# Kernel optimization log

Hardware: AMD Instinct MI355X
Metric: run time of the kernel (lower is better)

Reference implementation:

```python
import jax, jax.numpy as jnp
import numpy as np
import math

HEADS = 8


def rope(t):
    # t: [..., seq, dim]; lucidrains-style interleaved rotary embedding
    seq, dim = t.shape[-2], t.shape[-1]
    inv = 1.0 / (10000.0 ** (jnp.arange(0, dim, 2, dtype=jnp.float32) / dim))
    freqs = jnp.arange(seq, dtype=jnp.float32)[:, None] * inv[None, :]  # [seq, dim/2]
    freqs = jnp.repeat(freqs, 2, axis=-1)                               # [seq, dim]
    cos, sin = jnp.cos(freqs), jnp.sin(freqs)
    t2 = t.reshape(t.shape[:-1] + (dim // 2, 2))
    rot = jnp.stack([-t2[..., 1], t2[..., 0]], axis=-1).reshape(t.shape)
    return t * cos + rot * sin


def conv1x3(x, w):
    # x: [b,c,h,w], w: [out_c,in_c,1,3], padding (0,1), no bias
    return jax.lax.conv_general_dilated(
        x, w, window_strides=(1, 1), padding=((0, 0), (1, 1)),
        dimension_numbers=('NCHW', 'OIHW', 'NCHW'))


def mcl_pw(x, w_pw):
    # per-channel linear on feature axis h: w_pw [c, out_f, in_f]
    return jnp.einsum('bchw,cgh->bcgw', x, w_pw)


def setup_inputs() -> dict:
    key = jax.random.key(0)
    ks = jax.random.split(key, 10)
    b, c, f, w = 2, 8, 256, 1024
    s = 0.05
    return {
        'x': jax.random.normal(ks[0], (b, c, f, w), dtype=jnp.float32),
        'q_pw': jax.random.normal(ks[1], (c, f, f), dtype=jnp.float32) * s,
        'q_cw': jax.random.normal(ks[2], (c, c, 1, 3), dtype=jnp.float32) * s,
        'k_pw': jax.random.normal(ks[3], (c, f, f), dtype=jnp.float32) * s,
        'k_cw': jax.random.normal(ks[4], (c, c, 1, 3), dtype=jnp.float32) * s,
        'v_pw': jax.random.normal(ks[5], (c, f, f), dtype=jnp.float32) * s,
        'v_cw': jax.random.normal(ks[6], (c, c, 1, 3), dtype=jnp.float32) * s,
        'out_pw': jax.random.normal(ks[7], (c, f, f), dtype=jnp.float32) * s,
        'out_dw': jax.random.normal(ks[8], (c, c), dtype=jnp.float32) * s,
    }


def reference(x, q_pw, q_cw, k_pw, k_cw, v_pw, v_cw, out_pw, out_dw):
    b, c, h, w = x.shape
    hd = h // HEADS

    def split_heads(y):  # [b,c,h,w] -> [b,c,heads,w,hd]
        return y.transpose(0, 1, 3, 2).reshape(b, c, w, HEADS, hd).transpose(0, 1, 3, 2, 4)

    q = rope(split_heads(conv1x3(mcl_pw(x, q_pw), q_cw)))
    k = rope(split_heads(conv1x3(mcl_pw(x, k_pw), k_cw)))
    v = split_heads(conv1x3(mcl_pw(x, v_pw), v_cw))

    # non-standard scaling by sqrt(h) = sqrt(features)
    qk = jnp.einsum('bcnqd,bcnkd->bcnqk', q, k) / math.sqrt(h)
    a = jnp.einsum('bcnqk,bcnkd->bcnqd', jax.nn.softmax(qk, axis=-1), v)
    a = a.transpose(0, 1, 3, 2, 4).reshape(b, c, w, h).transpose(0, 1, 3, 2)  # [b,c,h,w]

    # out_proj: depthwise channel mix then per-channel positionwise linear
    out = jnp.einsum('bchw,dc->bdhw', a, out_dw)
    out = mcl_pw(out, out_pw)
    return out
```

## Files before the change

### kernel.cpp

```cpp
#include <hip/hip_runtime.h>
#include <hip/hip_bf16.h>

#define B 2
#define C 8
#define F 256
#define W 1024
#define NH 8
#define HD 32

typedef float f32x4 __attribute__((ext_vector_type(4)));
typedef short sh8 __attribute__((ext_vector_type(8)));
typedef short sh4 __attribute__((ext_vector_type(4)));
typedef unsigned short u16;

static __device__ __forceinline__ u16 f2b(float x) {
  union { __hip_bfloat16 h; u16 u; } v;
  v.h = __float2bfloat16(x);
  return v.u;
}
static __device__ __forceinline__ float b2f(u16 x) {
  union { unsigned int u; float f; } v;
  v.u = ((unsigned int)x) << 16;
  return v.f;
}
static __device__ __forceinline__ float ubits(unsigned int u) {
  union { unsigned int u; float f; } v;
  v.u = u;
  return v.f;
}

static __device__ __forceinline__ f32x4 mfma32(sh8 a, sh8 b, f32x4 c) {
  return __builtin_amdgcn_mfma_f32_16x16x32_bf16(a, b, c, 0, 0, 0);
}

static __device__ __forceinline__ f32x4 mfma16(sh4 a, sh4 b, f32x4 c) {
#if __has_builtin(__builtin_amdgcn_mfma_f32_16x16x16bf16_1k)
  return __builtin_amdgcn_mfma_f32_16x16x16bf16_1k(a, b, c, 0, 0, 0);
#else
  f32x4 d;
  asm("v_mfma_f32_16x16x16_bf16 %0, %1, %2, %3" : "=v"(d) : "v"(a), "v"(b), "v"(c));
  return d;
#endif
}

static __device__ __forceinline__ void gload16(const u16* g, u16* l, int ln) {
#if __has_builtin(__builtin_amdgcn_global_load_lds)
  __builtin_amdgcn_global_load_lds((const __attribute__((address_space(1))) void*)g,
                                   (__attribute__((address_space(3))) void*)l, 16, 0, 0);
#else
  *(sh8*)(l + ln * 8) = *(const sh8*)g;
#endif
}

__global__ __launch_bounds__(256) void cvt4(const float* __restrict__ s0, const float* __restrict__ s1,
                                            const float* __restrict__ s2, const float* __restrict__ s3,
                                            u16* __restrict__ d0, u16* __restrict__ d1,
                                            u16* __restrict__ d2, u16* __restrict__ d3, int n4) {
  const int which = blockIdx.y;
  const float* s = which == 0 ? s0 : which == 1 ? s1 : which == 2 ? s2 : s3;
  u16* d = which == 0 ? d0 : which == 1 ? d1 : which == 2 ? d2 : d3;
  const int i = blockIdx.x * 256 + threadIdx.x;
  if (i < n4) {
    const float4 v = reinterpret_cast<const float4*>(s)[i];
    union { u16 h[4]; uint2 u; } o;
    o.h[0] = f2b(v.x); o.h[1] = f2b(v.y); o.h[2] = f2b(v.z); o.h[3] = f2b(v.w);
    reinterpret_cast<uint2*>(d)[i] = o.u;
  }
}

__global__ __launch_bounds__(256) void rope_tab_k(float2* __restrict__ TAB) {
  const int idx = blockIdx.x * 256 + threadIdx.x;
  const int j = idx >> 10, w = idx & 1023;
  const float inv = powf(10000.f, -(float)(2 * j) / 32.f);
  float sn, cs;
  sincosf((float)w * inv, &sn, &cs);
  TAB[idx] = make_float2(cs, sn);
}

__global__ __launch_bounds__(256) void xt_k(const float* __restrict__ x,
                                            u16* __restrict__ xt) {
  const int bc = blockIdx.z, h0 = blockIdx.y * 32, w0 = blockIdx.x * 32;
  const int t = threadIdx.x;
  __shared__ u16 sm[32][34];
  const int a = t & 31, bql = t >> 5;
  const float* src = x + ((size_t)bc * F + h0) * W + w0;
#pragma unroll
  for (int p = 0; p < 4; ++p) {
    const int hl = bql + p * 8;
    sm[a][hl] = f2b(src[(size_t)hl * W + a]);
  }
  __syncthreads();
  u16* dst = xt + ((size_t)bc * W + w0) * F + h0;
#pragma unroll
  for (int p = 0; p < 4; ++p) {
    const int wl = bql + p * 8;
    dst[(size_t)wl * F + a] = sm[wl][a];
  }
}

template <bool OUTBF>
__global__ __launch_bounds__(256) void gemm_bt(const u16* __restrict__ Aw,
                                               const u16* __restrict__ Bt,
                                               void* __restrict__ Cc) {
  const int bc = blockIdx.z;
  const int proj = blockIdx.y >> 1;
  const int g0 = (blockIdx.y & 1) * 128;
  const int w0 = blockIdx.x * 64;
  const int t = threadIdx.x;
  const int ln = t & 63, wid = t >> 6;
  const int lr = ln & 15, lk = (ln >> 4) * 8;
  const int wr = wid >> 1, wc = wid & 1;

  const u16* Ab = Aw + (size_t)proj * C * F * F + (size_t)(bc & 7) * F * F;
  const u16* Bb = Bt + (size_t)bc * W * F;

  __shared__ u16 sA[16 * 512];
  __shared__ u16 sB[8 * 512];

  const u16* ga0 = Ab + (size_t)(g0 + (wid * 2 + 0) * 16 + lr) * F + lk;
  const u16* ga1 = Ab + (size_t)(g0 + (wid * 2 + 1) * 16 + lr) * F + lk;
  const u16* gb0 = Bb + (size_t)(w0 + wid * 16 + lr) * F + lk;

  f32x4 acc[4][2] = {};

  for (int h0 = 0; h0 < F; h0 += 64) {
    __syncthreads();
    gload16(ga0 + h0,      &sA[(0 * 8 + wid * 2 + 0) * 512], ln);
    gload16(ga0 + h0 + 32, &sA[(1 * 8 + wid * 2 + 0) * 512], ln);
    gload16(ga1 + h0,      &sA[(0 * 8 + wid * 2 + 1) * 512], ln);
    gload16(ga1 + h0 + 32, &sA[(1 * 8 + wid * 2 + 1) * 512], ln);
    gload16(gb0 + h0,      &sB[(0 * 4 + wid) * 512], ln);
    gload16(gb0 + h0 + 32, &sB[(1 * 4 + wid) * 512], ln);
    __syncthreads();
#pragma unroll
    for (int kh = 0; kh < 2; ++kh) {
      sh8 af[4], bfr[2];
#pragma unroll
      for (int mi = 0; mi < 4; ++mi)
        af[mi] = *(const sh8*)&sA[((kh * 8 + wr * 4 + mi) * 64 + ln) * 8];
#pragma unroll
      for (int ni = 0; ni < 2; ++ni)
        bfr[ni] = *(const sh8*)&sB[((kh * 4 + wc * 2 + ni) * 64 + ln) * 8];
#pragma unroll
      for (int mi = 0; mi < 4; ++mi)
#pragma unroll
        for (int ni = 0; ni < 2; ++ni)
          acc[mi][ni] = mfma32(af[mi], bfr[ni], acc[mi][ni]);
    }
  }

  const int lq = ln >> 4;
  const size_t cbase = ((size_t)proj * B * C + bc) * F * W;
  if (OUTBF) {
    u16* Cb = (u16*)Cc + cbase;
#pragma unroll
    for (int mi = 0; mi < 4; ++mi)
#pragma unroll
      for (int ni = 0; ni < 2; ++ni)
#pragma unroll
        for (int r = 0; r < 4; ++r)
          Cb[(size_t)(g0 + wr * 64 + mi * 16 + lq * 4 + r) * W + w0 + wc * 32 + ni * 16 + lr] =
              f2b(acc[mi][ni][r]);
  } else {
    float* Cb = (float*)Cc + cbase;
#pragma unroll
    for (int mi = 0; mi < 4; ++mi)
#pragma unroll
      for (int ni = 0; ni < 2; ++ni)
#pragma unroll
        for (int r = 0; r < 4; ++r)
          Cb[(size_t)(g0 + wr * 64 + mi * 16 + lq * 4 + r) * W + w0 + wc * 32 + ni * 16 + lr] =
              acc[mi][ni][r];
  }
}

__global__ __launch_bounds__(256) void conv2(const u16* __restrict__ IN,
                                             const float* __restrict__ CWq,
                                             const float* __restrict__ CWk,
                                             const float* __restrict__ CWv,
                                             const float* __restrict__ TAB,
                                             u16* __restrict__ OUT) {
  const int f2 = blockIdx.x;
  const int z = blockIdx.y;
  const int proj = z >> 1, b = z & 1;
  const float* CW = proj == 0 ? CWq : proj == 1 ? CWk : CWv;
  const size_t NB = (size_t)B * C * F * W;
  const u16* INp = IN + (size_t)proj * NB;
  u16* OUTp = OUT + (size_t)proj * NB;
  const int do_rope = (proj < 2);
  const float scale = (proj == 0) ? 0.0625f : 1.0f;
  const int f0 = f2 * 2;
  const int t = threadIdx.x;

  __shared__ u16 s[2][C][1040];
  __shared__ float cw[C][C][3];
  if (t < C * C * 3) ((float*)cw)[t] = CW[t];
  if (t < 16) {
    const int fi = t >> 3, c2 = t & 7;
    s[fi][c2][7] = 0;
    s[fi][c2][1032] = 0;
  }
  {
    const int l = t & 127, rsel = t >> 7;
#pragma unroll
    for (int p = 0; p < 8; ++p) {
      const int row = p * 2 + rsel;
      const int fi = row >> 3, c2 = row & 7;
      const u16* src = INp + ((size_t)(b * C + c2) * F + f0 + fi) * W + l * 8;
      *(sh8*)&s[fi][c2][8 + l * 8] = *(const sh8*)src;
    }
  }
  __syncthreads();

  float acc[2][C][4] = {};
#pragma unroll
  for (int c = 0; c < C; ++c) {
    float v[2][6];
#pragma unroll
    for (int fi = 0; fi < 2; ++fi) {
      const unsigned int* r32 = (const unsigned int*)&s[fi][c][0];
      const unsigned int r0 = r32[2 * t + 3];
      const unsigned int r1 = r32[2 * t + 4];
      const unsigned int r2 = r32[2 * t + 5];
      const unsigned int r3 = r32[2 * t + 6];
      v[fi][0] = ubits(r0 & 0xffff0000u);
      v[fi][1] = ubits(r1 << 16);
      v[fi][2] = ubits(r1 & 0xffff0000u);
      v[fi][3] = ubits(r2 << 16);
      v[fi][4] = ubits(r2 & 0xffff0000u);
      v[fi][5] = ubits(r3 << 16);
    }
#pragma unroll
    for (int d = 0; d < C; ++d) {
      const float c0 = cw[d][c][0], c1 = cw[d][c][1], c2_ = cw[d][c][2];
#pragma unroll
      for (int fi = 0; fi < 2; ++fi)
#pragma unroll
        for (int o = 0; o < 4; ++o)
          acc[fi][d][o] += v[fi][o] * c0 + v[fi][o + 1] * c1 + v[fi][o + 2] * c2_;
    }
  }

  float cs[4] = {1.f, 1.f, 1.f, 1.f}, sn[4] = {0.f, 0.f, 0.f, 0.f};
  if (do_rope) {
    const int j = f2 & 15;
    const float4* tp = (const float4*)(TAB + (size_t)(j * 1024 + 4 * t) * 2);
    const float4 A0 = tp[0], A1 = tp[1];
    cs[0] = A0.x; sn[0] = A0.y; cs[1] = A0.z; sn[1] = A0.w;
    cs[2] = A1.x; sn[2] = A1.y; cs[3] = A1.z; sn[3] = A1.w;
  }

#pragma unroll
  for (int d = 0; d < C; ++d) {
    sh4 pk0, pk1;
#pragma unroll
    for (int o = 0; o < 4; ++o) {
      const float a0 = acc[0][d][o], a1 = acc[1][d][o];
      float o0 = a0, o1 = a1;
      if (do_rope) { o0 = a0 * cs[o] - a1 * sn[o]; o1 = a1 * cs[o] + a0 * sn[o]; }
      pk0[o] = (short)f2b(o0 * scale);
      pk1[o] = (short)f2b(o1 * scale);
    }
    u16* dst = OUTp + ((size_t)(b * C + d) * F + f0) * W + 4 * t;
    *(sh4*)dst = pk0;
    *(sh4*)(dst + W) = pk1;
  }
}

__global__ __launch_bounds__(256) void attn_bf(const u16* __restrict__ Q,
                                               const u16* __restrict__ K,
                                               const u16* __restrict__ Vv,
                                               float* __restrict__ O) {
  const int bc = blockIdx.z, n = blockIdx.y, q0 = blockIdx.x * 64;
  const int t = threadIdx.x, ln = t & 63, wid = t >> 6;
  const int lc = ln & 15, g4 = (ln >> 4) * 4;
  const int dq = (ln >> 4) * 8;
  const size_t base = ((size_t)bc * F + n * HD) * W;

  __shared__ u16 Kl[2][64 * 40];
  __shared__ u16 Vl[2][32 * 76];

  const int sk = t & 63, sdb = (t >> 6) * 8;
  const int sd = t >> 3, skc = (t & 7) * 8;
  const u16* gK = K + base + (size_t)sdb * W + sk;
  const u16* gV = Vv + base + (size_t)sd * W + skc;

  const int qw = q0 + wid * 16 + lc;
  sh8 qf;
#pragma unroll
  for (int j = 0; j < 8; ++j) qf[j] = (short)Q[base + (size_t)(dq + j) * W + qw];

  f32x4 o0 = {0.f, 0.f, 0.f, 0.f}, o1 = {0.f, 0.f, 0.f, 0.f};
  float lsum = 0.f;

  {
    sh8 hv;
#pragma unroll
    for (int j = 0; j < 8; ++j) hv[j] = (short)gK[(size_t)j * W];
    *(sh8*)&Kl[0][sk * 40 + sdb] = hv;
    *(sh8*)&Vl[0][sd * 76 + skc] = *(const sh8*)gV;
  }
  __syncthreads();

  for (int tile = 0; tile < 16; ++tile) {
    const int cur = tile & 1;
    sh8 hvK, hvV;
    if (tile < 15) {
      const int off = (tile + 1) * 64;
#pragma unroll
      for (int j = 0; j < 8; ++j) hvK[j] = (short)gK[(size_t)j * W + off];
      hvV = *(const sh8*)(gV + off);
    }

    f32x4 sf[4];
    __builtin_amdgcn_s_setprio(1);
#pragma unroll
    for (int kh = 0; kh < 4; ++kh) {
      const sh8 kf = *(const sh8*)&Kl[cur][(kh * 16 + lc) * 40 + dq];
      f32x4 z = {0.f, 0.f, 0.f, 0.f};
      sf[kh] = mfma32(kf, qf, z);
    }
    __builtin_amdgcn_s_setprio(0);

#pragma unroll
    for (int kh = 0; kh < 4; ++kh)
#pragma unroll
      for (int r = 0; r < 4; ++r) {
        const float pv = __expf(sf[kh][r]);
        sf[kh][r] = pv;
        lsum += pv;
      }

    __builtin_amdgcn_s_setprio(1);
#pragma unroll
    for (int kh = 0; kh < 4; ++kh) {
      const sh4 pb = {(short)f2b(sf[kh][0]), (short)f2b(sf[kh][1]),
                      (short)f2b(sf[kh][2]), (short)f2b(sf[kh][3])};
      const sh4 vf0 = *(const sh4*)&Vl[cur][lc * 76 + kh * 16 + g4];
      const sh4 vf1 = *(const sh4*)&Vl[cur][(16 + lc) * 76 + kh * 16 + g4];
      o0 = mfma16(pb, vf0, o0);
      o1 = mfma16(pb, vf1, o1);
    }
    __builtin_amdgcn_s_setprio(0);

    if (tile < 15) {
      *(sh8*)&Kl[cur ^ 1][sk * 40 + sdb] = hvK;
      *(sh8*)&Vl[cur ^ 1][sd * 76 + skc] = hvV;
    }
    __syncthreads();
  }

  lsum += __shfl_xor(lsum, 16);
  lsum += __shfl_xor(lsum, 32);
#pragma unroll
  for (int r = 0; r < 4; ++r) {
    const float inv = 1.f / __shfl(lsum, g4 + r);
    const int qrow = q0 + wid * 16 + g4 + r;
    O[base + (size_t)lc * W + qrow] = o0[r] * inv;
    O[base + (size_t)(16 + lc) * W + qrow] = o1[r] * inv;
  }
}

__global__ __launch_bounds__(256) void chanmix_t(const float* __restrict__ A,
                                                 const float* __restrict__ DW,
                                                 u16* __restrict__ O1) {
  const int b = blockIdx.z, f0 = blockIdx.y * 32, w0 = blockIdx.x * 32;
  const int t = threadIdx.x;
  __shared__ u16 sm[C][32][34];
  float dwv[C][C];
#pragma unroll
  for (int d = 0; d < C; ++d)
#pragma unroll
    for (int c = 0; c < C; ++c) dwv[d][c] = DW[d * C + c];

  const int wl = t & 31, fs = t >> 5;
#pragma unroll
  for (int p = 0; p < 4; ++p) {
    const int fl = p * 8 + fs;
    float av[C];
#pragma unroll
    for (int c = 0; c < C; ++c)
      av[c] = A[((size_t)(b * C + c) * F + f0 + fl) * W + w0 + wl];
#pragma unroll
    for (int d = 0; d < C; ++d) {
      float s = 0.f;
#pragma unroll
      for (int c = 0; c < C; ++c) s += av[c] * dwv[d][c];
      sm[d][wl][fl] = f2b(s);
    }
  }
  __syncthreads();
  const int fl2 = t & 31, ws = t >> 5;
#pragma unroll
  for (int d = 0; d < C; ++d)
#pragma unroll
    for (int p = 0; p < 4; ++p) {
      const int wl2 = p * 8 + ws;
      O1[((size_t)(b * C + d) * W + w0 + wl2) * F + f0 + fl2] = sm[d][wl2][fl2];
    }
}

extern "C" void kernel_launch(void* const* d_in, const int* in_sizes, int n_in,
                              void* d_out, int out_size, void* d_ws, size_t ws_size,
                              hipStream_t stream) {
  const float* x      = (const float*)d_in[0];
  const float* q_pw   = (const float*)d_in[1];
  const float* q_cw   = (const float*)d_in[2];
  const float* k_pw   = (const float*)d_in[3];
  const float* k_cw   = (const float*)d_in[4];
  const float* v_pw   = (const float*)d_in[5];
  const float* v_cw   = (const float*)d_in[6];
  const float* out_pw = (const float*)d_in[7];
  const float* out_dw = (const float*)d_in[8];

  const size_t NB = (size_t)B * C * F * W;
  const size_t CFF = (size_t)C * F * F;

  u16* xt   = (u16*)d_ws;
  u16* wqkv = xt + NB;
  u16* wo   = wqkv + 3 * CFF;
  u16* t0b  = wo + CFF;
  u16* qkvb = t0b + 3 * NB;
  float* tab = (float*)(qkvb + 3 * NB);
  float* obuf = (float*)t0b;
  u16* o1t  = xt;

  cvt4<<<dim3((int)(CFF / 4 + 255) / 256, 4), 256, 0, stream>>>(
      q_pw, k_pw, v_pw, out_pw, wqkv, wqkv + CFF, wqkv + 2 * CFF, wo, (int)(CFF / 4));
  rope_tab_k<<<64, 256, 0, stream>>>((float2*)tab);
  xt_k<<<dim3(W / 32, F / 32, B * C), 256, 0, stream>>>(x, xt);

  gemm_bt<true><<<dim3(W / 64, 6, B * C), 256, 0, stream>>>(wqkv, xt, t0b);
  conv2<<<dim3(F / 2, 3 * B), 256, 0, stream>>>(t0b, q_cw, k_cw, v_cw, tab, qkvb);

  attn_bf<<<dim3(W / 64, NH, B * C), 256, 0, stream>>>(qkvb, qkvb + NB, qkvb + 2 * NB, obuf);

  chanmix_t<<<dim3(W / 32, F / 32, B), 256, 0, stream>>>(obuf, out_dw, o1t);
  gemm_bt<false><<<dim3(W / 64, 2, B * C), 256, 0, stream>>>(wo, o1t, d_out);
}
```

Measured before the change: 120.8 us.

## Pre-transpose K for attention, use async LDS loads with swizzle and exp2 softmax

```diff
diff --git a/kernel.cpp b/kernel.cpp
--- a/kernel.cpp
+++ b/kernel.cpp
@@ -12,6 +12,8 @@
 typedef short sh8 __attribute__((ext_vector_type(8)));
 typedef short sh4 __attribute__((ext_vector_type(4)));
 typedef unsigned short u16;
+
+#define QSCALE 0.09016843880556021f
 
 static __device__ __forceinline__ u16 f2b(float x) {
   union { __hip_bfloat16 h; u16 u; } v;
@@ -188,7 +190,7 @@
   const u16* INp = IN + (size_t)proj * NB;
   u16* OUTp = OUT + (size_t)proj * NB;
   const int do_rope = (proj < 2);
-  const float scale = (proj == 0) ? 0.0625f : 1.0f;
+  const float scale = (proj == 0) ? QSCALE : 1.0f;
   const int f0 = f2 * 2;
   const int t = threadIdx.x;
 
@@ -267,8 +269,30 @@
   }
 }
 
+__global__ __launch_bounds__(256) void ktr(const u16* __restrict__ kb,
+                                           u16* __restrict__ kT) {
+  const int w0 = blockIdx.x * 64, n = blockIdx.y, bc = blockIdx.z;
+  const int t = threadIdx.x;
+  __shared__ u16 sm[64 * 40];
+  const u16* src = kb + ((size_t)bc * F + n * HD) * W;
+  {
+    const int wp = (t & 31) * 2;
+#pragma unroll
+    for (int p = 0; p < 4; ++p) {
+      const int d = p * 8 + (t >> 5);
+      const unsigned int val = *(const unsigned int*)(src + (size_t)d * W + w0 + wp);
+      sm[wp * 40 + d] = (u16)(val & 0xffffu);
+      sm[(wp + 1) * 40 + d] = (u16)(val >> 16);
+    }
+  }
+  __syncthreads();
+  const int key = t >> 2, di = (t & 3) * 8;
+  *(sh8*)(kT + ((size_t)(bc * NH + n) * W + w0 + key) * HD + di) =
+      *(const sh8*)&sm[key * 40 + di];
+}
+
 __global__ __launch_bounds__(256) void attn_bf(const u16* __restrict__ Q,
-                                               const u16* __restrict__ K,
+                                               const u16* __restrict__ KT,
                                                const u16* __restrict__ Vv,
                                                float* __restrict__ O) {
   const int bc = blockIdx.z, n = blockIdx.y, q0 = blockIdx.x * 64;
@@ -277,12 +301,13 @@
   const int dq = (ln >> 4) * 8;
   const size_t base = ((size_t)bc * F + n * HD) * W;
 
-  __shared__ u16 Kl[2][64 * 40];
+  __shared__ u16 Kl[2][64 * 32];
   __shared__ u16 Vl[2][32 * 76];
 
-  const int sk = t & 63, sdb = (t >> 6) * 8;
+  const int skey = t >> 2;
+  const int sdi = (t & 3) ^ ((skey >> 1) & 3);
+  const u16* gKT = KT + ((size_t)(bc * NH + n) * W + skey) * HD + sdi * 8;
   const int sd = t >> 3, skc = (t & 7) * 8;
-  const u16* gK = K + base + (size_t)sdb * W + sk;
   const u16* gV = Vv + base + (size_t)sd * W + skc;
 
   const int qw = q0 + wid * 16 + lc;
@@ -290,25 +315,23 @@
 #pragma unroll
   for (int j = 0; j < 8; ++j) qf[j] = (short)Q[base + (size_t)(dq + j) * W + qw];
 
+  const int krd = 8 * ((ln >> 4) ^ ((lc >> 1) & 3));
+
   f32x4 o0 = {0.f, 0.f, 0.f, 0.f}, o1 = {0.f, 0.f, 0.f, 0.f};
-  float lsum = 0.f;
+  float ls[4] = {0.f, 0.f, 0.f, 0.f};
 
   {
-    sh8 hv;
-#pragma unroll
-    for (int j = 0; j < 8; ++j) hv[j] = (short)gK[(size_t)j * W];
-    *(sh8*)&Kl[0][sk * 40 + sdb] = hv;
+    gload16(gKT, &Kl[0][wid * 512], ln);
     *(sh8*)&Vl[0][sd * 76 + skc] = *(const sh8*)gV;
   }
   __syncthreads();
 
   for (int tile = 0; tile < 16; ++tile) {
     const int cur = tile & 1;
-    sh8 hvK, hvV;
+    sh8 hvV;
     if (tile < 15) {
       const int off = (tile + 1) * 64;
-#pragma unroll
-      for (int j = 0; j < 8; ++j) hvK[j] = (short)gK[(size_t)j * W + off];
+      gload16(gKT + (size_t)off * HD, &Kl[cur ^ 1][wid * 512], ln);
       hvV = *(const sh8*)(gV + off);
     }
 
@@ -316,20 +339,21 @@
     __builtin_amdgcn_s_setprio(1);
 #pragma unroll
     for (int kh = 0; kh < 4; ++kh) {
-      const sh8 kf = *(const sh8*)&Kl[cur][(kh * 16 + lc) * 40 + dq];
+      const sh8 kf = *(const sh8*)&Kl[cur][(kh * 16 + lc) * 32 + krd];
       f32x4 z = {0.f, 0.f, 0.f, 0.f};
       sf[kh] = mfma32(kf, qf, z);
     }
     __builtin_amdgcn_s_setprio(0);
 
 #pragma unroll
-    for (int kh = 0; kh < 4; ++kh)
-#pragma unroll
-      for (int r = 0; r < 4; ++r) {
-        const float pv = __expf(sf[kh][r]);
-        sf[kh][r] = pv;
-        lsum += pv;
-      }
+    for (int kh = 0; kh < 4; ++kh) {
+      const float p0 = exp2f(sf[kh][0]);
+      const float p1 = exp2f(sf[kh][1]);
+      const float p2 = exp2f(sf[kh][2]);
+      const float p3 = exp2f(sf[kh][3]);
+      sf[kh][0] = p0; sf[kh][1] = p1; sf[kh][2] = p2; sf[kh][3] = p3;
+      ls[kh] += (p0 + p1) + (p2 + p3);
+    }
 
     __builtin_amdgcn_s_setprio(1);
 #pragma unroll
@@ -344,12 +368,12 @@
     __builtin_amdgcn_s_setprio(0);
 
     if (tile < 15) {
-      *(sh8*)&Kl[cur ^ 1][sk * 40 + sdb] = hvK;
       *(sh8*)&Vl[cur ^ 1][sd * 76 + skc] = hvV;
     }
     __syncthreads();
   }
 
+  float lsum = (ls[0] + ls[1]) + (ls[2] + ls[3]);
   lsum += __shfl_xor(lsum, 16);
   lsum += __shfl_xor(lsum, 32);
 #pragma unroll
@@ -423,6 +447,7 @@
   u16* qkvb = t0b + 3 * NB;
   float* tab = (float*)(qkvb + 3 * NB);
   float* obuf = (float*)t0b;
+  u16* kT   = t0b + 2 * NB;
   u16* o1t  = xt;
 
   cvt4<<<dim3((int)(CFF / 4 + 255) / 256, 4), 256, 0, stream>>>(
@@ -433,7 +458,9 @@
   gemm_bt<true><<<dim3(W / 64, 6, B * C), 256, 0, stream>>>(wqkv, xt, t0b);
   conv2<<<dim3(F / 2, 3 * B), 256, 0, stream>>>(t0b, q_cw, k_cw, v_cw, tab, qkvb);
 
-  attn_bf<<<dim3(W / 64, NH, B * C), 256, 0, stream>>>(qkvb, qkvb + NB, qkvb + 2 * NB, obuf);
+  ktr<<<dim3(W / 64, NH, B * C), 256, 0, stream>>>(qkvb + NB, kT);
+
+  attn_bf<<<dim3(W / 64, NH, B * C), 256, 0, stream>>>(qkvb, kT, qkvb + 2 * NB, obuf);
 
   chanmix_t<<<dim3(W / 32, F / 32, B), 256, 0, stream>>>(obuf, out_dw, o1t);
   gemm_bt<false><<<dim3(W / 64, 2, B * C), 256, 0, stream>>>(wo, o1t, d_out);
```

Measured after the change: 135.1 us. +11.8%, slower.
